# Performance work log

Hardware: AMD Instinct MI355X
Metric: run time of the kernel (lower is better)

## Reference

```python
import jax, jax.numpy as jnp
import numpy as np

B, N, ND, ED, TD, H = 4, 256, 256, 64, 64, 8
D = ND // H
SCALE = np.float32(1.0 / np.sqrt(ND))
EPS = 1e-5


def leaky(x):
    return jnp.where(x >= 0, x, 0.05 * x)


def _ln(x, g, b):
    m = x.mean(axis=-1, keepdims=True)
    v = ((x - m) ** 2).mean(axis=-1, keepdims=True)
    return (x - m) * jax.lax.rsqrt(v + EPS) * g + b


def setup_inputs() -> dict:
    key = jax.random.key(0)
    ks = iter(jax.random.split(key, 64))

    def w(shape):
        return (jax.random.normal(next(ks), shape, jnp.float32) * 0.02).astype(jnp.float32)

    inp = {
        'nodes': jax.random.normal(next(ks), (B, N, ND), jnp.float32),
        'edges': jax.random.normal(next(ks), (B, N, N, ED), jnp.float32),
        'times': jax.random.normal(next(ks), (B, TD), jnp.float32),
        'Wq': w((ND + TD, ND)), 'bq': w((ND,)),
        'Wk': w((ND + TD, ND)), 'bk': w((ND,)),
        'Wv': w((ND + TD, ND)), 'bv': w((ND,)),
        'Wm': w((ED, ND)), 'bm': w((ND,)),
        'Wa': w((ED, ND)), 'ba': w((ND,)),
        'Wno': w((ND, ND)), 'bno': w((ND,)),
        'Weo': w((ND, ED)), 'beo': w((ED,)),
        'ln1n_g': jnp.ones((ND,), jnp.float32), 'ln1n_b': jnp.zeros((ND,), jnp.float32),
        'ln1e_g': jnp.ones((ED,), jnp.float32), 'ln1e_b': jnp.zeros((ED,), jnp.float32),
        'Wn1': w((ND, ND)), 'bn1': w((ND,)),
        'Wn2': w((ND, ND)), 'bn2': w((ND,)),
        'We1': w((ED, ED)), 'be1': w((ED,)),
        'We2': w((ED, ED)), 'be2': w((ED,)),
        'ln2n_g': jnp.ones((ND,), jnp.float32), 'ln2n_b': jnp.zeros((ND,), jnp.float32),
        'ln2e_g': jnp.ones((ED,), jnp.float32), 'ln2e_b': jnp.zeros((ED,), jnp.float32),
    }
    return inp


def reference(nodes, edges, times, Wq, bq, Wk, bk, Wv, bv, Wm, bm, Wa, ba,
              Wno, bno, Weo, beo, ln1n_g, ln1n_b, ln1e_g, ln1e_b,
              Wn1, bn1, Wn2, bn2, We1, be1, We2, be2,
              ln2n_g, ln2n_b, ln2e_g, ln2e_b):
    b, n, _ = nodes.shape
    # concat time embedding onto every node: [B, N, ND+TD]
    nt = jnp.concatenate([nodes, jnp.broadcast_to(times[:, None, :], (b, n, times.shape[-1]))], axis=-1)
    q = (nt @ Wq + bq).reshape(b, n, H, D)
    k = (nt @ Wk + bk).reshape(b, n, H, D)
    # all-pairs elementwise qk product: [B, N, N, H, D]
    attn = q[:, :, None, :, :] * k[:, None, :, :, :] * SCALE
    em = (edges @ Wm + bm).reshape(b, n, n, H, D)
    ea = (edges @ Wa + ba).reshape(b, n, n, H, D)
    new_edges = attn * em + attn + ea                    # [B,N,N,H,D]
    a = jax.nn.softmax(new_edges.sum(axis=4), axis=2)    # [B,N,N,H]
    v = (nt @ Wv + bv).reshape(b, n, H, D)
    wv = jnp.einsum('bijh,bjhd->bihd', a, v).reshape(b, n, ND)
    ne_flat = new_edges.reshape(b, n, n, ND)
    attn_nodes = wv @ Wno + bno                          # lin_nodes_out
    attn_edges = leaky(ne_flat) @ Weo + beo              # lin_edges_out
    attn_nodes = leaky(_ln(attn_nodes + nodes, ln1n_g, ln1n_b))
    attn_edges = _ln(attn_edges + edges, ln1e_g, ln1e_b)
    mn = leaky(attn_nodes @ Wn1 + bn1) @ Wn2 + bn2
    me = leaky(attn_edges @ We1 + be1) @ We2 + be2
    out_nodes = leaky(_ln(mn + attn_nodes, ln2n_g, ln2n_b))
    out_edges = _ln(me + attn_edges, ln2e_g, ln2e_b)
    return out_nodes, out_edges
```

## Files before the change

### kernel.cpp

```cpp
#include <hip/hip_runtime.h>
#include <hip/hip_bf16.h>

#define DEVFN __device__ __forceinline__

static constexpr float KSCALE = 0.0625f;
static constexpr float KEPS   = 1e-5f;

static constexpr int WS_Q   = 0;
static constexpr int WS_K   = 262144;
static constexpr int WS_V   = 524288;
static constexpr int WS_WVO = 786432;
static constexpr int WS_WMT = 1048576;
static constexpr int WS_WAT = WS_WMT + 16384;
static constexpr int WS_WEO = WS_WAT + 16384;
static constexpr int WS_WE1 = WS_WEO + 16384;
static constexpr int WS_WE2 = WS_WE1 + 4096;
static constexpr int WS_WQ  = WS_WE2 + 4096;
static constexpr int WS_WK  = WS_WQ + 81920;
static constexpr int WS_WVW = WS_WK + 81920;
static constexpr int WS_WNO = WS_WVW + 81920;
static constexpr int WS_WN1 = WS_WNO + 65536;
static constexpr int WS_WN2 = WS_WN1 + 65536;
static constexpr int WS_P   = WS_WN2 + 65536;
static constexpr int P_BQ=0, P_BK=256, P_BV=512, P_BM=768, P_BA=1024, P_BNO=1280,
  P_BEO=1536, P_LN1NG=1600, P_LN1NB=1856, P_LN1EG=2112, P_LN1EB=2176,
  P_BN1=2240, P_BN2=2496, P_BE1=2752, P_BE2=2816, P_LN2NG=2880, P_LN2NB=3136,
  P_LN2EG=3392, P_LN2EB=3456;
static constexpr int WS_BF  = WS_P + 3520;
static constexpr int WS_KT  = WS_BF + 28672;

typedef __attribute__((ext_vector_type(8))) short short8v;
typedef __attribute__((ext_vector_type(4))) float f32x4;
#define MFMA16(a, b, c) __builtin_amdgcn_mfma_f32_16x16x32_bf16((a), (b), (c), 0, 0, 0)

DEVFN float ldin(const void* p, int i, int bf) {
  if (bf) {
    unsigned short u = ((const unsigned short*)p)[i];
    return __uint_as_float(((unsigned)u) << 16);
  }
  return ((const float*)p)[i];
}
DEVFN unsigned short f2bf(float x) {
  unsigned b = __float_as_uint(x);
  b += 0x7FFFu + ((b >> 16) & 1u);
  return (unsigned short)(b >> 16);
}
DEVFN float bf2f(unsigned short u) { return __uint_as_float(((unsigned)u) << 16); }
DEVFN float lrelu(float x) { return x >= 0.f ? x : 0.05f * x; }
DEVFN int   dtflag(const void* l1ng) {
  return (((const unsigned*)l1ng)[0] != 0x3F800000u) ? 1 : 0;
}
DEVFN unsigned pack_bf2(float a, float b) {
  return ((unsigned)f2bf(b) << 16) | (unsigned)f2bf(a);
}

__global__ __launch_bounds__(256) void k0_prep(float* __restrict__ wsf,
    const void* Wq, const void* bq, const void* Wk, const void* bk,
    const void* Wv, const void* bv, const void* Wm, const void* bm,
    const void* Wa, const void* ba, const void* Wno, const void* bno,
    const void* Weo, const void* beo, const void* l1ng, const void* l1nb,
    const void* l1eg, const void* l1eb, const void* Wn1, const void* bn1,
    const void* Wn2, const void* bn2, const void* We1, const void* be1,
    const void* We2, const void* be2, const void* l2ng, const void* l2nb,
    const void* l2eg, const void* l2eb)
{
  const int bf = dtflag(l1ng);
  const int g  = blockIdx.x * blockDim.x + threadIdx.x;
  const int gs = gridDim.x * blockDim.x;
  short* sb = (short*)(wsf + WS_BF);
#define CPY(src, off, n) for (int i = g; i < (n); i += gs) wsf[(off) + i] = ldin(src, i, bf)
  for (int i = g; i < 16384; i += gs) {
    int c = i >> 6, t = i & 63;
    sb[i]         = (short)f2bf(ldin(Wm, t * 256 + c, bf));
    sb[16384 + i] = (short)f2bf(ldin(Wa, t * 256 + c, bf));
  }
  for (int i = g; i < 16384; i += gs) {
    int u = i >> 8, c = i & 255;
    sb[32768 + i] = (short)f2bf(ldin(Weo, c * 64 + u, bf));
  }
  for (int i = g; i < 4096; i += gs) {
    int u = i >> 6, t = i & 63;
    sb[49152 + i] = (short)f2bf(ldin(We1, t * 64 + u, bf));
    sb[53248 + i] = (short)f2bf(ldin(We2, t * 64 + u, bf));
  }
  CPY(Wq, WS_WQ, 81920);
  CPY(Wk, WS_WK, 81920);
  CPY(Wv, WS_WVW, 81920);
  CPY(Wno, WS_WNO, 65536);
  CPY(Wn1, WS_WN1, 65536);
  CPY(Wn2, WS_WN2, 65536);
  CPY(bq,  WS_P + P_BQ, 256);   CPY(bk,  WS_P + P_BK, 256);
  CPY(bv,  WS_P + P_BV, 256);   CPY(bm,  WS_P + P_BM, 256);
  CPY(ba,  WS_P + P_BA, 256);   CPY(bno, WS_P + P_BNO, 256);
  CPY(beo, WS_P + P_BEO, 64);
  CPY(l1ng, WS_P + P_LN1NG, 256); CPY(l1nb, WS_P + P_LN1NB, 256);
  CPY(l1eg, WS_P + P_LN1EG, 64);  CPY(l1eb, WS_P + P_LN1EB, 64);
  CPY(bn1, WS_P + P_BN1, 256);  CPY(bn2, WS_P + P_BN2, 256);
  CPY(be1, WS_P + P_BE1, 64);   CPY(be2, WS_P + P_BE2, 64);
  CPY(l2ng, WS_P + P_LN2NG, 256); CPY(l2nb, WS_P + P_LN2NB, 256);
  CPY(l2eg, WS_P + P_LN2EG, 64);  CPY(l2eb, WS_P + P_LN2EB, 64);
#undef CPY
}

__global__ __launch_bounds__(256) void k1_qkv(float* __restrict__ wsf,
    const void* nodes, const void* times, const void* l1ng)
{
  const int bf  = dtflag(l1ng);
  const int bid = blockIdx.x;
  const int b   = bid >> 8;
  const int n   = bid & 255;
  const int c   = threadIdx.x;
  __shared__ float nt[320];
  nt[c] = ldin(nodes, bid * 256 + c, bf);
  if (c < 64) nt[256 + c] = ldin(times, b * 64 + c, bf);
  __syncthreads();
  const float* Pb = wsf + WS_P;
  float aq = Pb[P_BQ + c], ak = Pb[P_BK + c], av = Pb[P_BV + c];
  const float* wq = wsf + WS_WQ  + c;
  const float* wk = wsf + WS_WK  + c;
  const float* wv = wsf + WS_WVW + c;
  for (int t = 0; t < 320; ++t) {
    float x = nt[t];
    aq = fmaf(x, wq[t << 8], aq);
    ak = fmaf(x, wk[t << 8], ak);
    av = fmaf(x, wv[t << 8], av);
  }
  wsf[WS_Q + bid * 256 + c] = aq * KSCALE;
  wsf[WS_KT + b * 65536 + c * 256 + n] = ak;
  wsf[WS_V + bid * 256 + c] = av;
}

__global__ __launch_bounds__(256, 2) void k2_edges(float* __restrict__ wsf,
    const void* edges, void* __restrict__ out, const void* l1ng)
{
  const int bf  = dtflag(l1ng);
  const int bid = blockIdx.x;
  const int b   = bid >> 8;
  const int tid = threadIdx.x;
  const int wv_ = tid >> 6;
  const int l   = tid & 63;
  const int l15 = l & 15, gq = l >> 4;

  __shared__ float sl[8 * 256];
  __shared__ unsigned short ptile[4][4096];

  const float* Pb = wsf + WS_P;
  const short* WmTb  = (const short*)(wsf + WS_BF);
  const short* WaTb  = WmTb + 16384;
  const short* WeoTb = WaTb + 16384;
  const short* We1Tb = WeoTb + 16384;
  const short* We2Tb = We1Tb + 4096;
  const float* kTb   = wsf + WS_KT + b * 65536;

#pragma unroll
  for (int h = 0; h < 8; ++h) sl[(h << 8) + tid] = 0.f;

  short8v Ef[2][4];
#pragma unroll
  for (int jf = 0; jf < 4; ++jf) {
    const int jg = (wv_ << 6) + (jf << 4) + l15;
    const size_t ebase = (size_t)(bid * 256 + jg) * 64;
#pragma unroll
    for (int kb = 0; kb < 2; ++kb) {
      const int t0 = (kb << 5) + (gq << 3);
      if (bf) {
        Ef[kb][jf] = *(const short8v*)((const unsigned short*)edges + ebase + t0);
      } else {
        const float* ep = (const float*)edges + ebase + t0;
        const float4 x0 = *(const float4*)ep;
        const float4 x1 = *(const float4*)(ep + 4);
        typedef __attribute__((ext_vector_type(4))) unsigned uint4v;
        uint4v d;
        d[0] = pack_bf2(x0.x, x0.y); d[1] = pack_bf2(x0.z, x0.w);
        d[2] = pack_bf2(x1.x, x1.y); d[3] = pack_bf2(x1.z, x1.w);
        Ef[kb][jf] = __builtin_bit_cast(short8v, d);
      }
    }
  }

  f32x4 Oacc[4][4];
#pragma unroll
  for (int uf = 0; uf < 4; ++uf)
#pragma unroll
    for (int jf = 0; jf < 4; ++jf) { Oacc[uf][jf] = f32x4{0.f, 0.f, 0.f, 0.f}; }

  char* myp = (char*)&ptile[wv_][0];
  const int swz = (l15 & 7) << 4;

#pragma unroll 1
  for (int chunk = 0; chunk < 4; ++chunk) {
#pragma unroll
    for (int ci = 0; ci < 4; ++ci) {
      const int cf = (chunk << 2) + ci;
      const int crow = ((cf << 4) + l15) << 6;
      const short8v Am0 = *(const short8v*)(WmTb + crow + (gq << 3));
      const short8v Am1 = *(const short8v*)(WmTb + crow + 32 + (gq << 3));
      const short8v Aa0 = *(const short8v*)(WaTb + crow + (gq << 3));
      const short8v Aa1 = *(const short8v*)(WaTb + crow + 32 + (gq << 3));
      const int ce = (cf << 4) + (gq << 2);
      const float4 q4  = *(const float4*)(wsf + WS_Q + bid * 256 + ce);
      const float4 bm4 = *(const float4*)(Pb + P_BM + ce);
      const float4 ba4 = *(const float4*)(Pb + P_BA + ce);
      const int h = cf >> 1;
#pragma unroll
      for (int jf = 0; jf < 4; ++jf) {
        f32x4 em = f32x4{0.f, 0.f, 0.f, 0.f};
        f32x4 ea = f32x4{0.f, 0.f, 0.f, 0.f};
        em = MFMA16(Am0, Ef[0][jf], em);
        em = MFMA16(Am1, Ef[1][jf], em);
        ea = MFMA16(Aa0, Ef[0][jf], ea);
        ea = MFMA16(Aa1, Ef[1][jf], ea);
        const int jg = (wv_ << 6) + (jf << 4) + l15;
        const float kv0 = kTb[(ce + 0) * 256 + jg];
        const float kv1 = kTb[(ce + 1) * 256 + jg];
        const float kv2 = kTb[(ce + 2) * 256 + jg];
        const float kv3 = kTb[(ce + 3) * 256 + jg];
        const float ne0 = (q4.x * kv0) * (em[0] + bm4.x + 1.f) + (ea[0] + ba4.x);
        const float ne1 = (q4.y * kv1) * (em[1] + bm4.y + 1.f) + (ea[1] + ba4.y);
        const float ne2 = (q4.z * kv2) * (em[2] + bm4.z + 1.f) + (ea[2] + ba4.z);
        const float ne3 = (q4.w * kv3) * (em[3] + bm4.w + 1.f) + (ea[3] + ba4.w);
        float part = (ne0 + ne1) + (ne2 + ne3);
        part += __shfl_xor(part, 16, 64);
        part += __shfl_xor(part, 32, 64);
        if (gq == 0) sl[(h << 8) + jg] += part;
        const unsigned pd0 = pack_bf2(lrelu(ne0), lrelu(ne1));
        const unsigned pd1 = pack_bf2(lrelu(ne2), lrelu(ne3));
        const int jl = (jf << 4) + l15;
        const unsigned boff = (jl << 7) + ((unsigned)((ci << 5) + (gq << 3)) ^ swz);
        *(unsigned long long*)(myp + boff) = ((unsigned long long)pd1 << 32) | pd0;
      }
    }
    short8v Bp[2][4];
#pragma unroll
    for (int kb = 0; kb < 2; ++kb)
#pragma unroll
      for (int jf = 0; jf < 4; ++jf) {
        const int jl = (jf << 4) + l15;
        const unsigned boff = (jl << 7) + ((unsigned)((kb << 6) + (gq << 4)) ^ swz);
        Bp[kb][jf] = *(const short8v*)(myp + boff);
      }
#pragma unroll
    for (int uf = 0; uf < 4; ++uf) {
      const int urow = ((uf << 4) + l15) << 8;
      const int cb = chunk << 6;
      const short8v Aw0 = *(const short8v*)(WeoTb + urow + cb + (gq << 3));
      const short8v Aw1 = *(const short8v*)(WeoTb + urow + cb + 32 + (gq << 3));
#pragma unroll
      for (int jf = 0; jf < 4; ++jf) {
        Oacc[uf][jf] = MFMA16(Aw0, Bp[0][jf], Oacc[uf][jf]);
        Oacc[uf][jf] = MFMA16(Aw1, Bp[1][jf], Oacc[uf][jf]);
      }
    }
  }

#pragma unroll
  for (int uf = 0; uf < 4; ++uf)
#pragma unroll
    for (int jf = 0; jf < 4; ++jf) {
      const unsigned pd0 = pack_bf2(Oacc[uf][jf][0], Oacc[uf][jf][1]);
      const unsigned pd1 = pack_bf2(Oacc[uf][jf][2], Oacc[uf][jf][3]);
      const int jl = (jf << 4) + l15;
      const unsigned boff = (jl << 7) + ((unsigned)((uf << 5) + (gq << 3)) ^ swz);
      *(unsigned long long*)(myp + boff) = ((unsigned long long)pd1 << 32) | pd0;
    }

  __syncthreads();

  {
    const int h = tid >> 5, ll = tid & 31;
    float* row = sl + (h << 8);
    float pv[8];
    float m = -1e30f;
#pragma unroll
    for (int k2 = 0; k2 < 8; ++k2) { float x = row[ll + (k2 << 5)]; pv[k2] = x; m = fmaxf(m, x); }
#pragma unroll
    for (int off = 16; off; off >>= 1) m = fmaxf(m, __shfl_xor(m, off, 64));
    float sum = 0.f;
#pragma unroll
    for (int k2 = 0; k2 < 8; ++k2) { float p = __expf(pv[k2] - m); pv[k2] = p; sum += p; }
#pragma unroll
    for (int off = 16; off; off >>= 1) sum += __shfl_xor(sum, off, 64);
    const float inv = 1.f / sum;
#pragma unroll
    for (int k2 = 0; k2 < 8; ++k2) row[ll + (k2 << 5)] = pv[k2] * inv;
  }
  __syncthreads();

  {
    const int c = tid;
    const float* arow = sl + ((c >> 5) << 8);
    const float* vcol = wsf + WS_V + b * 65536 + c;
    float a0 = 0.f, a1 = 0.f, a2 = 0.f, a3 = 0.f;
    for (int jj = 0; jj < 256; jj += 4) {
      a0 = fmaf(arow[jj],     vcol[jj << 8],        a0);
      a1 = fmaf(arow[jj + 1], vcol[(jj + 1) << 8],  a1);
      a2 = fmaf(arow[jj + 2], vcol[(jj + 2) << 8],  a2);
      a3 = fmaf(arow[jj + 3], vcol[(jj + 3) << 8],  a3);
    }
    wsf[WS_WVO + bid * 256 + c] = (a0 + a1) + (a2 + a3);
  }

  const int jl   = tid & 63;
  const int rswz = (jl & 7) << 4;
  float e[64];
  {
    float o[64];
#pragma unroll
    for (int s = 0; s < 8; ++s) {
      const short8v v = *(const short8v*)(myp + (jl << 7) + ((unsigned)(s << 4) ^ rswz));
#pragma unroll
      for (int e2 = 0; e2 < 8; ++e2) o[(s << 3) + e2] = bf2f((unsigned short)v[e2]);
    }
    const size_t ebase = (size_t)(bid * 256 + tid) * 64;
    if (bf) {
      const unsigned short* ep = (const unsigned short*)edges + ebase;
#pragma unroll
      for (int t = 0; t < 64; ++t) e[t] = bf2f(ep[t]);
    } else {
      const float4* ep = (const float4*)((const float*)edges + ebase);
#pragma unroll
      for (int t = 0; t < 16; ++t) {
        const float4 v4 = ep[t];
        e[4*t] = v4.x; e[4*t+1] = v4.y; e[4*t+2] = v4.z; e[4*t+3] = v4.w;
      }
    }
#pragma unroll
    for (int u = 0; u < 64; ++u) o[u] = o[u] + Pb[P_BEO + u] + e[u];
    float mu = 0.f;
#pragma unroll
    for (int u = 0; u < 64; ++u) mu += o[u];
    mu *= (1.f / 64.f);
    float s2 = 0.f;
#pragma unroll
    for (int u = 0; u < 64; ++u) { float d = o[u] - mu; s2 = fmaf(d, d, s2); }
    const float rs = rsqrtf(s2 * (1.f / 64.f) + KEPS);
#pragma unroll
    for (int u = 0; u < 64; ++u) e[u] = fmaf((o[u] - mu) * rs, Pb[P_LN1EG + u], Pb[P_LN1EB + u]);
#pragma unroll
    for (int u0 = 0; u0 < 64; u0 += 4) {
      const unsigned pd0 = pack_bf2(e[u0],     e[u0 + 1]);
      const unsigned pd1 = pack_bf2(e[u0 + 2], e[u0 + 3]);
      *(unsigned long long*)(myp + (jl << 7) + ((unsigned)(u0 << 1) ^ rswz)) =
        ((unsigned long long)pd1 << 32) | pd0;
    }
  }

  {
    short8v Bf[2][4];
#pragma unroll
    for (int kb = 0; kb < 2; ++kb)
#pragma unroll
      for (int jf = 0; jf < 4; ++jf) {
        const int jfl = (jf << 4) + l15;
        Bf[kb][jf] = *(const short8v*)(myp + (jfl << 7) + ((unsigned)((kb << 6) + (gq << 4)) ^ swz));
      }
    f32x4 Hc[4][4];
#pragma unroll
    for (int uf = 0; uf < 4; ++uf) {
      const int ur = ((uf << 4) + l15) << 6;
      const short8v A0 = *(const short8v*)(We1Tb + ur + (gq << 3));
      const short8v A1 = *(const short8v*)(We1Tb + ur + 32 + (gq << 3));
#pragma unroll
      for (int jf = 0; jf < 4; ++jf) {
        f32x4 hh = f32x4{0.f, 0.f, 0.f, 0.f};
        hh = MFMA16(A0, Bf[0][jf], hh);
        hh = MFMA16(A1, Bf[1][jf], hh);
        Hc[uf][jf] = hh;
      }
    }
#pragma unroll
    for (int uf = 0; uf < 4; ++uf) {
      const int u0 = (uf << 4) + (gq << 2);
      const float4 b14 = *(const float4*)(Pb + P_BE1 + u0);
#pragma unroll
      for (int jf = 0; jf < 4; ++jf) {
        const int jfl = (jf << 4) + l15;
        const unsigned pd0 = pack_bf2(lrelu(Hc[uf][jf][0] + b14.x), lrelu(Hc[uf][jf][1] + b14.y));
        const unsigned pd1 = pack_bf2(lrelu(Hc[uf][jf][2] + b14.z), lrelu(Hc[uf][jf][3] + b14.w));
        *(unsigned long long*)(myp + (jfl << 7) + ((unsigned)((uf << 5) + (gq << 3)) ^ swz)) =
          ((unsigned long long)pd1 << 32) | pd0;
      }
    }
#pragma unroll
    for (int kb = 0; kb < 2; ++kb)
#pragma unroll
      for (int jf = 0; jf < 4; ++jf) {
        const int jfl = (jf << 4) + l15;
        Bf[kb][jf] = *(const short8v*)(myp + (jfl << 7) + ((unsigned)((kb << 6) + (gq << 4)) ^ swz));
      }
#pragma unroll
    for (int uf = 0; uf < 4; ++uf) {
      const int ur = ((uf << 4) + l15) << 6;
      const short8v A0 = *(const short8v*)(We2Tb + ur + (gq << 3));
      const short8v A1 = *(const short8v*)(We2Tb + ur + 32 + (gq << 3));
      const int u0 = (uf << 4) + (gq << 2);
      const float4 b24 = *(const float4*)(Pb + P_BE2 + u0);
#pragma unroll
      for (int jf = 0; jf < 4; ++jf) {
        f32x4 mm = f32x4{0.f, 0.f, 0.f, 0.f};
        mm = MFMA16(A0, Bf[0][jf], mm);
        mm = MFMA16(A1, Bf[1][jf], mm);
        const int jfl = (jf << 4) + l15;
        const unsigned pd0 = pack_bf2(mm[0] + b24.x, mm[1] + b24.y);
        const unsigned pd1 = pack_bf2(mm[2] + b24.z, mm[3] + b24.w);
        *(unsigned long long*)(myp + (jfl << 7) + ((unsigned)((uf << 5) + (gq << 3)) ^ swz)) =
          ((unsigned long long)pd1 << 32) | pd0;
      }
    }
  }

  {
    float o[64];
#pragma unroll
    for (int s = 0; s < 8; ++s) {
      const short8v v = *(const short8v*)(myp + (jl << 7) + ((unsigned)(s << 4) ^ rswz));
#pragma unroll
      for (int e2 = 0; e2 < 8; ++e2) o[(s << 3) + e2] = bf2f((unsigned short)v[e2]);
    }
#pragma unroll
    for (int u = 0; u < 64; ++u) o[u] += e[u];
    float mu = 0.f;
#pragma unroll
    for (int u = 0; u < 64; ++u) mu += o[u];
    mu *= (1.f / 64.f);
    float s2 = 0.f;
#pragma unroll
    for (int u = 0; u < 64; ++u) { float d = o[u] - mu; s2 = fmaf(d, d, s2); }
    const float rs = rsqrtf(s2 * (1.f / 64.f) + KEPS);
    if (bf) {
      unsigned* op = (unsigned*)((unsigned short*)out + 262144 + (size_t)(bid * 256 + tid) * 64);
#pragma unroll
      for (int u = 0; u < 64; u += 2) {
        const float y0 = fmaf((o[u]     - mu) * rs, Pb[P_LN2EG + u],     Pb[P_LN2EB + u]);
        const float y1 = fmaf((o[u + 1] - mu) * rs, Pb[P_LN2EG + u + 1], Pb[P_LN2EB + u + 1]);
        op[u >> 1] = ((unsigned)f2bf(y1) << 16) | (unsigned)f2bf(y0);
      }
    } else {
      float4* op = (float4*)((float*)out + 262144 + (size_t)(bid * 256 + tid) * 64);
#pragma unroll
      for (int u = 0; u < 64; u += 4) {
        float4 y;
        y.x = fmaf((o[u]     - mu) * rs, Pb[P_LN2EG + u],     Pb[P_LN2EB + u]);
        y.y = fmaf((o[u + 1] - mu) * rs, Pb[P_LN2EG + u + 1], Pb[P_LN2EB + u + 1]);
        y.z = fmaf((o[u + 2] - mu) * rs, Pb[P_LN2EG + u + 2], Pb[P_LN2EB + u + 2]);
        y.w = fmaf((o[u + 3] - mu) * rs, Pb[P_LN2EG + u + 3], Pb[P_LN2EB + u + 3]);
        op[u >> 2] = y;
      }
    }
  }
}

DEVFN void bstats256(float v, float* red, float& mu, float& rs) {
  float s = v, q = v * v;
#pragma unroll
  for (int off = 32; off; off >>= 1) { s += __shfl_xor(s, off, 64); q += __shfl_xor(q, off, 64); }
  const int w = threadIdx.x >> 6;
  if ((threadIdx.x & 63) == 0) { red[w] = s; red[8 + w] = q; }
  __syncthreads();
  s = red[0] + red[1] + red[2] + red[3];
  q = red[8] + red[9] + red[10] + red[11];
  __syncthreads();
  mu = s * (1.f / 256.f);
  const float var = q * (1.f / 256.f) - mu * mu;
  rs = rsqrtf(var + KEPS);
}

__global__ __launch_bounds__(256) void k3_nodes(const float* __restrict__ wsf,
    const void* nodes, void* __restrict__ out, const void* l1ng)
{
  const int bf  = dtflag(l1ng);
  const int bid = blockIdx.x;
  const int c   = threadIdx.x;
  __shared__ float sh[256];
  __shared__ float red[16];
  const float* Pb = wsf + WS_P;

  sh[c] = wsf[WS_WVO + bid * 256 + c];
  __syncthreads();
  float an = Pb[P_BNO + c];
  {
    const float* w = wsf + WS_WNO + c;
    for (int t = 0; t < 256; ++t) an = fmaf(sh[t], w[t << 8], an);
  }
  an += ldin(nodes, bid * 256 + c, bf);
  float mu, rs;
  bstats256(an, red, mu, rs);
  float anf = lrelu(fmaf((an - mu) * rs, Pb[P_LN1NG + c], Pb[P_LN1NB + c]));
  __syncthreads();
  sh[c] = anf;
  __syncthreads();
  float h1 = Pb[P_BN1 + c];
  {
    const float* w = wsf + WS_WN1 + c;
    for (int t = 0; t < 256; ++t) h1 = fmaf(sh[t], w[t << 8], h1);
  }
  h1 = lrelu(h1);
  __syncthreads();
  sh[c] = h1;
  __syncthreads();
  float mn = Pb[P_BN2 + c];
  {
    const float* w = wsf + WS_WN2 + c;
    for (int t = 0; t < 256; ++t) mn = fmaf(sh[t], w[t << 8], mn);
  }
  const float x2 = mn + anf;
  bstats256(x2, red, mu, rs);
  const float y = lrelu(fmaf((x2 - mu) * rs, Pb[P_LN2NG + c], Pb[P_LN2NB + c]));
  if (bf) ((unsigned short*)out)[bid * 256 + c] = f2bf(y);
  else    ((float*)out)[bid * 256 + c] = y;
}

extern "C" void kernel_launch(void* const* d_in, const int* in_sizes, int n_in,
                              void* d_out, int out_size, void* d_ws, size_t ws_size,
                              hipStream_t stream) {
  (void)in_sizes; (void)n_in; (void)out_size; (void)ws_size;
  float* wsf = (float*)d_ws;
  const void* nodes = d_in[0];
  const void* edges = d_in[1];
  const void* times = d_in[2];
  const void* l1ng  = d_in[17];

  k0_prep<<<128, 256, 0, stream>>>(wsf,
      d_in[3],  d_in[4],  d_in[5],  d_in[6],  d_in[7],  d_in[8],
      d_in[9],  d_in[10], d_in[11], d_in[12], d_in[13], d_in[14],
      d_in[15], d_in[16], d_in[17], d_in[18], d_in[19], d_in[20],
      d_in[21], d_in[22], d_in[23], d_in[24], d_in[25], d_in[26],
      d_in[27], d_in[28], d_in[29], d_in[30], d_in[31], d_in[32]);
  k1_qkv<<<1024, 256, 0, stream>>>(wsf, nodes, times, l1ng);
  k2_edges<<<1024, 256, 0, stream>>>(wsf, edges, d_out, l1ng);
  k3_nodes<<<1024, 256, 0, stream>>>(wsf, nodes, d_out, l1ng);
}
```

Before: 227.5 us.

## Compute QKV projection with bf16 MFMA and store Q, K, V transposed

The QKV projection in k1 moves from a scalar fp32 FMA loop (one block per node) to bf16 MFMA tiles. Each block now computes 16 nodes by 256 channels for one of the Q, K or V matrices, using weights pre-transposed to bf16 in k0. Q, K and V are all written in channel-major (transposed) layout. k2 now reads Q with strided scalar loads and reads V with contiguous float4 loads in the attention-weighted sum. This trades fp32 precision in the projections for tensor-core throughput and adds strided Q reads in the edge kernel.

```diff
diff --git a/kernel.cpp b/kernel.cpp
--- a/kernel.cpp
+++ b/kernel.cpp
@@ -27,10 +27,10 @@
   P_BN1=2240, P_BN2=2496, P_BE1=2752, P_BE2=2816, P_LN2NG=2880, P_LN2NB=3136,
   P_LN2EG=3392, P_LN2EB=3456;
 static constexpr int WS_BF  = WS_P + 3520;
-static constexpr int WS_KT  = WS_BF + 28672;
 
 typedef __attribute__((ext_vector_type(8))) short short8v;
 typedef __attribute__((ext_vector_type(4))) float f32x4;
+typedef __attribute__((ext_vector_type(4))) unsigned uint4v;
 #define MFMA16(a, b, c) __builtin_amdgcn_mfma_f32_16x16x32_bf16((a), (b), (c), 0, 0, 0)
 
 DEVFN float ldin(const void* p, int i, int bf) {
@@ -52,6 +52,14 @@
 }
 DEVFN unsigned pack_bf2(float a, float b) {
   return ((unsigned)f2bf(b) << 16) | (unsigned)f2bf(a);
+}
+DEVFN short8v pack8(const float* p) {
+  const float4 x0 = *(const float4*)p;
+  const float4 x1 = *(const float4*)(p + 4);
+  uint4v d;
+  d[0] = pack_bf2(x0.x, x0.y); d[1] = pack_bf2(x0.z, x0.w);
+  d[2] = pack_bf2(x1.x, x1.y); d[3] = pack_bf2(x1.z, x1.w);
+  return __builtin_bit_cast(short8v, d);
 }
 
 __global__ __launch_bounds__(256) void k0_prep(float* __restrict__ wsf,
@@ -83,9 +91,13 @@
     sb[49152 + i] = (short)f2bf(ldin(We1, t * 64 + u, bf));
     sb[53248 + i] = (short)f2bf(ldin(We2, t * 64 + u, bf));
   }
-  CPY(Wq, WS_WQ, 81920);
-  CPY(Wk, WS_WK, 81920);
-  CPY(Wv, WS_WVW, 81920);
+  for (int i = g; i < 81920; i += gs) {
+    int c = i / 320, t = i - c * 320;
+    const int src = t * 256 + c;
+    sb[57344 + i]  = (short)f2bf(ldin(Wq, src, bf));
+    sb[139264 + i] = (short)f2bf(ldin(Wk, src, bf));
+    sb[221184 + i] = (short)f2bf(ldin(Wv, src, bf));
+  }
   CPY(Wno, WS_WNO, 65536);
   CPY(Wn1, WS_WN1, 65536);
   CPY(Wn2, WS_WN2, 65536);
@@ -107,27 +119,64 @@
 {
   const int bf  = dtflag(l1ng);
   const int bid = blockIdx.x;
-  const int b   = bid >> 8;
-  const int n   = bid & 255;
-  const int c   = threadIdx.x;
-  __shared__ float nt[320];
-  nt[c] = ldin(nodes, bid * 256 + c, bf);
-  if (c < 64) nt[256 + c] = ldin(times, b * 64 + c, bf);
-  __syncthreads();
+  const int b   = bid / 48;
+  const int rem = bid - b * 48;
+  const int mat = rem >> 4;
+  const int n16 = rem & 15;
+  const int tid = threadIdx.x;
+  const int wv_ = tid >> 6;
+  const int l   = tid & 63;
+  const int l15 = l & 15, gq = l >> 4;
+
   const float* Pb = wsf + WS_P;
-  float aq = Pb[P_BQ + c], ak = Pb[P_BK + c], av = Pb[P_BV + c];
-  const float* wq = wsf + WS_WQ  + c;
-  const float* wk = wsf + WS_WK  + c;
-  const float* wv = wsf + WS_WVW + c;
-  for (int t = 0; t < 320; ++t) {
-    float x = nt[t];
-    aq = fmaf(x, wq[t << 8], aq);
-    ak = fmaf(x, wk[t << 8], ak);
-    av = fmaf(x, wv[t << 8], av);
-  }
-  wsf[WS_Q + bid * 256 + c] = aq * KSCALE;
-  wsf[WS_KT + b * 65536 + c * 256 + n] = ak;
-  wsf[WS_V + bid * 256 + c] = av;
+  const short* At = (const short*)(wsf + WS_BF) + 57344 + mat * 81920;
+  const int n = (n16 << 4) + l15;
+
+  short8v Bn[10];
+  if (bf) {
+    const unsigned short* np = (const unsigned short*)nodes + (size_t)(b * 256 + n) * 256;
+#pragma unroll
+    for (int kb = 0; kb < 8; ++kb)
+      Bn[kb] = *(const short8v*)(np + (kb << 5) + (gq << 3));
+    const unsigned short* tp = (const unsigned short*)times + b * 64;
+#pragma unroll
+    for (int kb = 8; kb < 10; ++kb)
+      Bn[kb] = *(const short8v*)(tp + ((kb - 8) << 5) + (gq << 3));
+  } else {
+    const float* np = (const float*)nodes + (size_t)(b * 256 + n) * 256;
+#pragma unroll
+    for (int kb = 0; kb < 8; ++kb)
+      Bn[kb] = pack8(np + (kb << 5) + (gq << 3));
+    const float* tp = (const float*)times + b * 64;
+#pragma unroll
+    for (int kb = 8; kb < 10; ++kb)
+      Bn[kb] = pack8(tp + ((kb - 8) << 5) + (gq << 3));
+  }
+
+  f32x4 acc[4];
+#pragma unroll
+  for (int cf = 0; cf < 4; ++cf) acc[cf] = f32x4{0.f, 0.f, 0.f, 0.f};
+#pragma unroll
+  for (int cf = 0; cf < 4; ++cf) {
+    const int crow = ((wv_ << 6) + (cf << 4) + l15) * 320;
+#pragma unroll
+    for (int kb = 0; kb < 10; ++kb) {
+      const short8v A = *(const short8v*)(At + crow + (kb << 5) + (gq << 3));
+      acc[cf] = MFMA16(A, Bn[kb], acc[cf]);
+    }
+  }
+
+  const int pbias = (mat == 0) ? P_BQ : (mat == 1 ? P_BK : P_BV);
+  float* dst = wsf + ((mat == 0) ? WS_Q : (mat == 1 ? WS_K : WS_V)) + b * 65536;
+  const float scale = (mat == 0) ? KSCALE : 1.f;
+#pragma unroll
+  for (int cf = 0; cf < 4; ++cf) {
+#pragma unroll
+    for (int r = 0; r < 4; ++r) {
+      const int c = (wv_ << 6) + (cf << 4) + (gq << 2) + r;
+      dst[c * 256 + n] = (acc[cf][r] + Pb[pbias + c]) * scale;
+    }
+  }
 }
 
 __global__ __launch_bounds__(256, 2) void k2_edges(float* __restrict__ wsf,
@@ -136,6 +185,7 @@
   const int bf  = dtflag(l1ng);
   const int bid = blockIdx.x;
   const int b   = bid >> 8;
+  const int i_  = bid & 255;
   const int tid = threadIdx.x;
   const int wv_ = tid >> 6;
   const int l   = tid & 63;
@@ -150,7 +200,8 @@
   const short* WeoTb = WaTb + 16384;
   const short* We1Tb = WeoTb + 16384;
   const short* We2Tb = We1Tb + 4096;
-  const float* kTb   = wsf + WS_KT + b * 65536;
+  const float* qTb   = wsf + WS_Q + b * 65536;
+  const float* kTb   = wsf + WS_K + b * 65536;
 
 #pragma unroll
   for (int h = 0; h < 8; ++h) sl[(h << 8) + tid] = 0.f;
@@ -166,14 +217,7 @@
       if (bf) {
         Ef[kb][jf] = *(const short8v*)((const unsigned short*)edges + ebase + t0);
       } else {
-        const float* ep = (const float*)edges + ebase + t0;
-        const float4 x0 = *(const float4*)ep;
-        const float4 x1 = *(const float4*)(ep + 4);
-        typedef __attribute__((ext_vector_type(4))) unsigned uint4v;
-        uint4v d;
-        d[0] = pack_bf2(x0.x, x0.y); d[1] = pack_bf2(x0.z, x0.w);
-        d[2] = pack_bf2(x1.x, x1.y); d[3] = pack_bf2(x1.z, x1.w);
-        Ef[kb][jf] = __builtin_bit_cast(short8v, d);
+        Ef[kb][jf] = pack8((const float*)edges + ebase + t0);
       }
     }
   }
@@ -198,7 +242,10 @@
       const short8v Aa0 = *(const short8v*)(WaTb + crow + (gq << 3));
       const short8v Aa1 = *(const short8v*)(WaTb + crow + 32 + (gq << 3));
       const int ce = (cf << 4) + (gq << 2);
-      const float4 q4  = *(const float4*)(wsf + WS_Q + bid * 256 + ce);
+      const float q0 = qTb[(ce + 0) * 256 + i_];
+      const float q1 = qTb[(ce + 1) * 256 + i_];
+      const float q2 = qTb[(ce + 2) * 256 + i_];
+      const float q3 = qTb[(ce + 3) * 256 + i_];
       const float4 bm4 = *(const float4*)(Pb + P_BM + ce);
       const float4 ba4 = *(const float4*)(Pb + P_BA + ce);
       const int h = cf >> 1;
@@ -215,10 +262,10 @@
         const float kv1 = kTb[(ce + 1) * 256 + jg];
         const float kv2 = kTb[(ce + 2) * 256 + jg];
         const float kv3 = kTb[(ce + 3) * 256 + jg];
-        const float ne0 = (q4.x * kv0) * (em[0] + bm4.x + 1.f) + (ea[0] + ba4.x);
-        const float ne1 = (q4.y * kv1) * (em[1] + bm4.y + 1.f) + (ea[1] + ba4.y);
-        const float ne2 = (q4.z * kv2) * (em[2] + bm4.z + 1.f) + (ea[2] + ba4.z);
-        const float ne3 = (q4.w * kv3) * (em[3] + bm4.w + 1.f) + (ea[3] + ba4.w);
+        const float ne0 = (q0 * kv0) * (em[0] + bm4.x + 1.f) + (ea[0] + ba4.x);
+        const float ne1 = (q1 * kv1) * (em[1] + bm4.y + 1.f) + (ea[1] + ba4.y);
+        const float ne2 = (q2 * kv2) * (em[2] + bm4.z + 1.f) + (ea[2] + ba4.z);
+        const float ne3 = (q3 * kv3) * (em[3] + bm4.w + 1.f) + (ea[3] + ba4.w);
         float part = (ne0 + ne1) + (ne2 + ne3);
         part += __shfl_xor(part, 16, 64);
         part += __shfl_xor(part, 32, 64);
@@ -289,13 +336,14 @@
   {
     const int c = tid;
     const float* arow = sl + ((c >> 5) << 8);
-    const float* vcol = wsf + WS_V + b * 65536 + c;
+    const float* vrow = wsf + WS_V + b * 65536 + c * 256;
     float a0 = 0.f, a1 = 0.f, a2 = 0.f, a3 = 0.f;
     for (int jj = 0; jj < 256; jj += 4) {
-      a0 = fmaf(arow[jj],     vcol[jj << 8],        a0);
-      a1 = fmaf(arow[jj + 1], vcol[(jj + 1) << 8],  a1);
-      a2 = fmaf(arow[jj + 2], vcol[(jj + 2) << 8],  a2);
-      a3 = fmaf(arow[jj + 3], vcol[(jj + 3) << 8],  a3);
+      const float4 v4 = *(const float4*)(vrow + jj);
+      a0 = fmaf(arow[jj],     v4.x, a0);
+      a1 = fmaf(arow[jj + 1], v4.y, a1);
+      a2 = fmaf(arow[jj + 2], v4.z, a2);
+      a3 = fmaf(arow[jj + 3], v4.w, a3);
     }
     wsf[WS_WVO + bid * 256 + c] = (a0 + a1) + (a2 + a3);
   }
@@ -526,7 +574,7 @@
       d_in[15], d_in[16], d_in[17], d_in[18], d_in[19], d_in[20],
       d_in[21], d_in[22], d_in[23], d_in[24], d_in[25], d_in[26],
       d_in[27], d_in[28], d_in[29], d_in[30], d_in[31], d_in[32]);
-  k1_qkv<<<1024, 256, 0, stream>>>(wsf, nodes, times, l1ng);
+  k1_qkv<<<192, 256, 0, stream>>>(wsf, nodes, times, l1ng);
   k2_edges<<<1024, 256, 0, stream>>>(wsf, edges, d_out, l1ng);
   k3_nodes<<<1024, 256, 0, stream>>>(wsf, nodes, d_out, l1ng);
 }
```

Measured after the change: 229.1 us. No clear change (+0.7%).
